# Kernel optimization log

Measured on AMD Instinct MI355X. Metric: run time of the kernel, lower is better.

Reference implementation:

```python
import jax, jax.numpy as jnp
import numpy as np

EPS = 1e-5

def _conv1x1(x, w, b):
    # x: [B, Din, N], w: [Dout, Din], b: [Dout]
    return jnp.einsum('od,bdn->bon', w, x) + b[None, :, None]

def _layernorm_last(x):
    # LayerNorm over last axis, no affine (matches torch LayerNorm([N], elementwise_affine=False))
    mu = jnp.mean(x, axis=-1, keepdims=True)
    var = jnp.mean(jnp.square(x - mu), axis=-1, keepdims=True)
    return (x - mu) * jax.lax.rsqrt(var + EPS)

def setup_inputs() -> dict:
    key = jax.random.key(0)
    ks = jax.random.split(key, 16)
    B, D, N, M = 1, 64, 64 * 80, 4096
    H2 = 2 * D
    s = 0.05
    return {
        'fea_pixel': jax.random.normal(ks[0], (B, D, N), jnp.float32),
        'fea_keypoint': jax.random.normal(ks[1], (B, D, M), jnp.float32),
        'Wq': jax.random.normal(ks[2], (D, D), jnp.float32) * s,
        'bq': jax.random.normal(ks[3], (D,), jnp.float32) * s,
        'Wk': jax.random.normal(ks[4], (D, D), jnp.float32) * s,
        'bk': jax.random.normal(ks[5], (D,), jnp.float32) * s,
        'Wv': jax.random.normal(ks[6], (D, D), jnp.float32) * s,
        'bv': jax.random.normal(ks[7], (D,), jnp.float32) * s,
        'Wm': jax.random.normal(ks[8], (D, D), jnp.float32) * s,
        'bm': jax.random.normal(ks[9], (D,), jnp.float32) * s,
        'W1': jax.random.normal(ks[10], (H2, D), jnp.float32) * s,
        'b1': jax.random.normal(ks[11], (H2,), jnp.float32) * s,
        'W2': jax.random.normal(ks[12], (D, H2), jnp.float32) * s,
        'b2': jax.random.normal(ks[13], (D,), jnp.float32) * s,
    }

def reference(fea_pixel, fea_keypoint, Wq, bq, Wk, bk, Wv, bv, Wm, bm, W1, b1, W2, b2):
    B, D, N = fea_pixel.shape
    num_heads = 4
    hd = D // num_heads  # head dim

    # QKV 1x1-conv projections, then split channels as (head_dim, num_heads) -- matches torch view
    q = _conv1x1(fea_pixel, Wq, bq).reshape(B, hd, num_heads, N)
    k = _conv1x1(fea_keypoint, Wk, bk).reshape(B, hd, num_heads, -1)
    v = _conv1x1(fea_keypoint, Wv, bv).reshape(B, hd, num_heads, -1)

    scores = jnp.einsum('bdhn,bdhm->bhnm', q, k) / jnp.sqrt(jnp.float32(hd))
    prob = jax.nn.softmax(scores, axis=-1)
    x = jnp.einsum('bhnm,bdhm->bdhn', prob, v)  # [B, hd, H, N]
    attn = _conv1x1(x.reshape(B, D, N), Wm, bm)

    fea = _layernorm_last(fea_pixel + attn)  # [B, D, N]

    # MLP over channel dim: operate on [B, N, D]
    y = jnp.swapaxes(fea, 1, 2)
    h = jax.nn.relu(jnp.einsum('bnd,od->bno', y, W1) + b1)
    m = jax.nn.relu(jnp.einsum('bno,do->bnd', h, W2) + b2)

    return _layernorm_last(fea + jnp.swapaxes(m, 1, 2))
```

## Files before the change

kernel.cpp:

```cpp
#include <hip/hip_runtime.h>
#include <hip/hip_bf16.h>

typedef __attribute__((ext_vector_type(4))) short short4v;
typedef __attribute__((ext_vector_type(4))) float float4v;

#define NHEADS 4
#define DMODEL 64
#define EPSV 1e-5f
#define QSCALE 0.36067376022224085f

__device__ inline short bf16rn(float f) {
    __hip_bfloat16 h = __float2bfloat16(f);
    return __builtin_bit_cast(short, h);
}

__device__ inline float exp2fast(float x) { return __builtin_amdgcn_exp2f(x); }

__global__ __launch_bounds__(512)
void proj_all_k(const float* __restrict__ Wk, const float* __restrict__ bk,
                const float* __restrict__ Wv, const float* __restrict__ bv,
                const float* __restrict__ Wq, const float* __restrict__ bq,
                const float* __restrict__ fkey, const float* __restrict__ fpix,
                short4v* __restrict__ kfrag, short4v* __restrict__ vfrag,
                short4v* __restrict__ qfrag, int M, int N) {
    __shared__ float xs[64][64];
    __shared__ float wsm[64][65];
    const int t = threadIdx.x;
    const int kvblocks = M >> 6;
    const bool isKV = (int)blockIdx.x < kvblocks;
    const int c0 = (isKV ? blockIdx.x : blockIdx.x - kvblocks) * 64;
    const float* x = isKV ? fkey : fpix;
    const int NC = isKV ? M : N;

    for (int i = t; i < 64 * 64; i += 512) {
        xs[i >> 6][i & 63] = x[(size_t)(i >> 6) * NC + c0 + (i & 63)];
        if (isKV) wsm[i >> 6][i & 63] = Wv[i];
    }
    __syncthreads();
    const int CT = NC >> 4;

    {
        const float* W = isKV ? Wk : Wq;
        const float* b = isKV ? bk : bq;
        const float scale = isKV ? 1.f : QSCALE;
        short4v* outf = isKV ? kfrag : qfrag;
        const int mm = t & 63;
        const int g8 = __builtin_amdgcn_readfirstlane(t >> 6);
        const int qd = g8 >> 1;
        const int half = g8 & 1;
        const int m = c0 + mm;
        float acc[8];
        #pragma unroll
        for (int a = 0; a < 8; ++a)
            acc[a] = b[qd * 16 + (a >> 1) * 4 + half * 2 + (a & 1)];
        #pragma unroll 8
        for (int d = 0; d < 64; ++d) {
            float xv = xs[d][mm];
            #pragma unroll
            for (int a = 0; a < 8; ++a)
                acc[a] = fmaf(W[(qd * 16 + (a >> 1) * 4 + half * 2 + (a & 1)) * 64 + d],
                              xv, acc[a]);
        }
        #pragma unroll
        for (int hh = 0; hh < 2; ++hh) {
            const int h = half * 2 + hh;
            short4v pk;
            #pragma unroll
            for (int j = 0; j < 4; ++j) pk[j] = bf16rn(acc[j * 2 + hh] * scale);
            outf[((size_t)(h * CT + (m >> 4))) * 64 + (m & 15) + 16 * qd] = pk;
        }
    }
    if (isKV) {
        const int lane = t & 63;
        const int w8 = t >> 6;
        const int d = lane >> 2, h = lane & 3;
        const float b0 = bv[lane];
        #pragma unroll
        for (int r = 0; r < 2; ++r) {
            const int mg = r * 8 + w8;
            float a0 = b0, a1 = b0, a2 = b0, a3 = b0;
            #pragma unroll 8
            for (int dd = 0; dd < 64; ++dd) {
                float wv = wsm[lane][dd];
                float4 xv = *(const float4*)&xs[dd][mg * 4];
                a0 = fmaf(wv, xv.x, a0); a1 = fmaf(wv, xv.y, a1);
                a2 = fmaf(wv, xv.z, a2); a3 = fmaf(wv, xv.w, a3);
            }
            short4v pk;
            pk[0] = bf16rn(a0); pk[1] = bf16rn(a1); pk[2] = bf16rn(a2); pk[3] = bf16rn(a3);
            const int m0 = c0 + mg * 4;
            vfrag[((size_t)(h * CT + (m0 >> 4))) * 64 + d + 16 * ((m0 >> 2) & 3)] = pk;
        }
    }
}

__global__ __launch_bounds__(256)
void attn_mfma_k(const short4v* __restrict__ qf, const short4v* __restrict__ kf,
                 const short4v* __restrict__ vf, float* __restrict__ xatt,
                 int N, int M) {
    const int lane = threadIdx.x & 63;
    const int ck = threadIdx.x >> 6;
    const int nt = blockIdx.x;
    const int h = blockIdx.y;
    const int NT = N >> 4, MT = M >> 4;
    const int mtN = MT >> 2;
    const int mt0 = ck * mtN;

    const short4v q4 = qf[((size_t)(h * NT + nt)) * 64 + lane];
    const float4v zero4 = {0.f, 0.f, 0.f, 0.f};
    float4v O = zero4;
    float ld = 0.f;
    const int g4 = (lane >> 4) << 2;

    const short4v* kp = kf + ((size_t)(h * MT + mt0)) * 64 + lane;
    const short4v* vp = vf + ((size_t)(h * MT + mt0)) * 64 + lane;
    for (int it = 0; it < mtN; it += 4) {
        short4v ka[4], va[4];
        #pragma unroll
        for (int u = 0; u < 4; ++u) {
            ka[u] = kp[(it + u) * 64];
            va[u] = vp[(it + u) * 64];
        }
        #pragma unroll
        for (int u = 0; u < 4; ++u) {
            float4v s = __builtin_amdgcn_mfma_f32_16x16x16bf16_1k(ka[u], q4, zero4, 0, 0, 0);
            float p0 = exp2fast(s[0]), p1 = exp2fast(s[1]),
                  p2 = exp2fast(s[2]), p3 = exp2fast(s[3]);
            ld += (p0 + p1) + (p2 + p3);
            short4v pa;
            pa[0] = bf16rn(p0); pa[1] = bf16rn(p1); pa[2] = bf16rn(p2); pa[3] = bf16rn(p3);
            O = __builtin_amdgcn_mfma_f32_16x16x16bf16_1k(pa, va[u], O, 0, 0, 0);
        }
    }
    ld += __shfl_xor(ld, 16);
    ld += __shfl_xor(ld, 32);

    __shared__ float Osm[4][256];
    __shared__ float lsm[4][16];
    #pragma unroll
    for (int b = 0; b < 4; ++b)
        Osm[ck][(g4 + b) * 16 + (lane & 15)] = O[b];
    if (lane < 16) lsm[ck][lane] = ld;
    __syncthreads();

    const int t = threadIdx.x;
    const int d = t >> 4, q = t & 15;
    const float L = (lsm[0][q] + lsm[1][q]) + (lsm[2][q] + lsm[3][q]);
    const int oi = q * 16 + d;
    const float val = (Osm[0][oi] + Osm[1][oi]) + (Osm[2][oi] + Osm[3][oi]);
    xatt[(size_t)(d * NHEADS + h) * N + nt * 16 + q] = val / L;
}

template<int DIN, int DOUT, bool RELU>
__global__ __launch_bounds__(256)
void conv1x1_k(const float* __restrict__ W, const float* __restrict__ bias,
               const float* __restrict__ x, float* __restrict__ out, int N) {
    __shared__ float xs[DIN][64];
    const int tid = threadIdx.x;
    const int n0 = blockIdx.x * 64;
    for (int i = tid; i < DIN * 64; i += 256) {
        int d = i >> 6, nn = i & 63;
        xs[d][nn] = x[(size_t)d * N + n0 + nn];
    }
    __syncthreads();
    const int nn = tid & 63;
    const int og = __builtin_amdgcn_readfirstlane((int)(threadIdx.x >> 6));
    const int ow = blockIdx.y * 16 + og * 4;
    float acc[4];
    #pragma unroll
    for (int i = 0; i < 4; ++i) acc[i] = bias[ow + i];
    #pragma unroll 8
    for (int d = 0; d < DIN; ++d) {
        float xv = xs[d][nn];
        #pragma unroll
        for (int i = 0; i < 4; ++i)
            acc[i] = fmaf(W[(ow + i) * DIN + d], xv, acc[i]);
    }
    #pragma unroll
    for (int i = 0; i < 4; ++i) {
        float r = RELU ? fmaxf(acc[i], 0.f) : acc[i];
        out[(size_t)(ow + i) * N + n0 + nn] = r;
    }
}

__global__ __launch_bounds__(512)
void add_ln_k(const float* __restrict__ a, const float* __restrict__ b,
              float* __restrict__ out, int N) {
    const int d = blockIdx.x;
    const int tid = threadIdx.x;
    const int nv = N >> 2;
    const float4* a4 = (const float4*)(a + (size_t)d * N);
    const float4* b4 = (const float4*)(b + (size_t)d * N);
    float4* o4 = (float4*)(out + (size_t)d * N);
    float s1 = 0.f, s2 = 0.f;
    for (int i = tid; i < nv; i += 512) {
        float4 va = a4[i], vb = b4[i];
        float tx = va.x + vb.x, ty = va.y + vb.y, tz = va.z + vb.z, tw = va.w + vb.w;
        s1 += (tx + ty) + (tz + tw);
        s2 = fmaf(tx, tx, s2); s2 = fmaf(ty, ty, s2);
        s2 = fmaf(tz, tz, s2); s2 = fmaf(tw, tw, s2);
    }
    #pragma unroll
    for (int m = 1; m < 64; m <<= 1) {
        s1 += __shfl_xor(s1, m);
        s2 += __shfl_xor(s2, m);
    }
    __shared__ float ws1[8], ws2[8];
    const int w = tid >> 6;
    if ((tid & 63) == 0) { ws1[w] = s1; ws2[w] = s2; }
    __syncthreads();
    s1 = 0.f; s2 = 0.f;
    #pragma unroll
    for (int i = 0; i < 8; ++i) { s1 += ws1[i]; s2 += ws2[i]; }
    const float mean = s1 / (float)N;
    const float var  = s2 / (float)N - mean * mean;
    const float rstd = rsqrtf(var + EPSV);
    for (int i = tid; i < nv; i += 512) {
        float4 va = a4[i], vb = b4[i];
        float4 r;
        r.x = (va.x + vb.x - mean) * rstd;
        r.y = (va.y + vb.y - mean) * rstd;
        r.z = (va.z + vb.z - mean) * rstd;
        r.w = (va.w + vb.w - mean) * rstd;
        o4[i] = r;
    }
}

extern "C" void kernel_launch(void* const* d_in, const int* in_sizes, int n_in,
                              void* d_out, int out_size, void* d_ws, size_t ws_size,
                              hipStream_t stream) {
    const float* fpix = (const float*)d_in[0];
    const float* fkey = (const float*)d_in[1];
    const float* Wq = (const float*)d_in[2];  const float* bq = (const float*)d_in[3];
    const float* Wk = (const float*)d_in[4];  const float* bk = (const float*)d_in[5];
    const float* Wv = (const float*)d_in[6];  const float* bv = (const float*)d_in[7];
    const float* Wm = (const float*)d_in[8];  const float* bm = (const float*)d_in[9];
    const float* W1 = (const float*)d_in[10]; const float* b1 = (const float*)d_in[11];
    const float* W2 = (const float*)d_in[12]; const float* b2 = (const float*)d_in[13];
    float* outp = (float*)d_out;

    const int N = in_sizes[0] / DMODEL;
    const int M = in_sizes[1] / DMODEL;

    char* wsb = (char*)d_ws;
    short4v* qfrag = (short4v*)(wsb);
    short4v* kfrag = (short4v*)(wsb + 655360);
    short4v* vfrag = (short4v*)(wsb + 1179648);
    float*   xatt  = (float*)(wsb + 1703936);
    float*   fea   = (float*)(wsb + 3014656);
    float*   attnb = (float*)(wsb + 4325376);
    float*   hbuf  = (float*)(wsb + 5636096);
    float*   mbuf  = (float*)(wsb + 8257536);

    proj_all_k<<<dim3(M / 64 + N / 64), 512, 0, stream>>>(Wk, bk, Wv, bv, Wq, bq,
                                                          fkey, fpix, kfrag, vfrag,
                                                          qfrag, M, N);
    attn_mfma_k<<<dim3(N / 16, NHEADS), 256, 0, stream>>>(qfrag, kfrag, vfrag, xatt, N, M);
    conv1x1_k<64, 64, false><<<dim3(N / 64, 4), 256, 0, stream>>>(Wm, bm, xatt, attnb, N);
    add_ln_k<<<64, 512, 0, stream>>>(fpix, attnb, fea, N);
    conv1x1_k<64, 128, true><<<dim3(N / 64, 8), 256, 0, stream>>>(W1, b1, fea, hbuf, N);
    conv1x1_k<128, 64, true><<<dim3(N / 64, 4), 256, 0, stream>>>(W2, b2, hbuf, mbuf, N);
    add_ln_k<<<64, 512, 0, stream>>>(fea, mbuf, outp, N);
}
```

Baseline: 62.36 us.

## Process two query tiles per wave in attention to reuse K/V fragments

Each wave in the attention kernel now computes two 16-row query tiles against the same K/V fragments, so every K/V load feeds four MFMAs instead of two. The block grows to 8 waves, each covering an eighth of the key range, and the grid halves along N. This cuts K/V memory traffic and adds independent MFMA work per iteration. In exchange it uses more registers and a larger shared-memory reduction over 8 partial sums.

Result: faster. 58.42 us (median of 2 runs) (-6.3%).

```diff
diff --git a/kernel.cpp b/kernel.cpp
--- a/kernel.cpp
+++ b/kernel.cpp
@@ -94,22 +94,23 @@
     }
 }
 
-__global__ __launch_bounds__(256)
+__global__ __launch_bounds__(512)
 void attn_mfma_k(const short4v* __restrict__ qf, const short4v* __restrict__ kf,
                  const short4v* __restrict__ vf, float* __restrict__ xatt,
                  int N, int M) {
     const int lane = threadIdx.x & 63;
     const int ck = threadIdx.x >> 6;
-    const int nt = blockIdx.x;
+    const int nt0 = blockIdx.x * 2;
     const int h = blockIdx.y;
     const int NT = N >> 4, MT = M >> 4;
-    const int mtN = MT >> 2;
+    const int mtN = MT >> 3;
     const int mt0 = ck * mtN;
 
-    const short4v q4 = qf[((size_t)(h * NT + nt)) * 64 + lane];
+    const short4v qa = qf[((size_t)(h * NT + nt0)) * 64 + lane];
+    const short4v qb = qf[((size_t)(h * NT + nt0 + 1)) * 64 + lane];
     const float4v zero4 = {0.f, 0.f, 0.f, 0.f};
-    float4v O = zero4;
-    float ld = 0.f;
+    float4v Oa = zero4, Ob = zero4;
+    float lda = 0.f, ldb = 0.f;
     const int g4 = (lane >> 4) << 2;
 
     const short4v* kp = kf + ((size_t)(h * MT + mt0)) * 64 + lane;
@@ -123,32 +124,48 @@
         }
         #pragma unroll
         for (int u = 0; u < 4; ++u) {
-            float4v s = __builtin_amdgcn_mfma_f32_16x16x16bf16_1k(ka[u], q4, zero4, 0, 0, 0);
-            float p0 = exp2fast(s[0]), p1 = exp2fast(s[1]),
-                  p2 = exp2fast(s[2]), p3 = exp2fast(s[3]);
-            ld += (p0 + p1) + (p2 + p3);
-            short4v pa;
-            pa[0] = bf16rn(p0); pa[1] = bf16rn(p1); pa[2] = bf16rn(p2); pa[3] = bf16rn(p3);
-            O = __builtin_amdgcn_mfma_f32_16x16x16bf16_1k(pa, va[u], O, 0, 0, 0);
-        }
-    }
-    ld += __shfl_xor(ld, 16);
-    ld += __shfl_xor(ld, 32);
-
-    __shared__ float Osm[4][256];
-    __shared__ float lsm[4][16];
-    #pragma unroll
-    for (int b = 0; b < 4; ++b)
-        Osm[ck][(g4 + b) * 16 + (lane & 15)] = O[b];
-    if (lane < 16) lsm[ck][lane] = ld;
+            float4v sa = __builtin_amdgcn_mfma_f32_16x16x16bf16_1k(ka[u], qa, zero4, 0, 0, 0);
+            float4v sb = __builtin_amdgcn_mfma_f32_16x16x16bf16_1k(ka[u], qb, zero4, 0, 0, 0);
+            float pa0 = exp2fast(sa[0]), pa1 = exp2fast(sa[1]),
+                  pa2 = exp2fast(sa[2]), pa3 = exp2fast(sa[3]);
+            float pb0 = exp2fast(sb[0]), pb1 = exp2fast(sb[1]),
+                  pb2 = exp2fast(sb[2]), pb3 = exp2fast(sb[3]);
+            lda += (pa0 + pa1) + (pa2 + pa3);
+            ldb += (pb0 + pb1) + (pb2 + pb3);
+            short4v fa, fb;
+            fa[0] = bf16rn(pa0); fa[1] = bf16rn(pa1); fa[2] = bf16rn(pa2); fa[3] = bf16rn(pa3);
+            fb[0] = bf16rn(pb0); fb[1] = bf16rn(pb1); fb[2] = bf16rn(pb2); fb[3] = bf16rn(pb3);
+            Oa = __builtin_amdgcn_mfma_f32_16x16x16bf16_1k(fa, va[u], Oa, 0, 0, 0);
+            Ob = __builtin_amdgcn_mfma_f32_16x16x16bf16_1k(fb, va[u], Ob, 0, 0, 0);
+        }
+    }
+    lda += __shfl_xor(lda, 16); lda += __shfl_xor(lda, 32);
+    ldb += __shfl_xor(ldb, 16); ldb += __shfl_xor(ldb, 32);
+
+    __shared__ float Osm[8][512];
+    __shared__ float lsm[8][32];
+    #pragma unroll
+    for (int b = 0; b < 4; ++b) {
+        Osm[ck][(g4 + b) * 16 + (lane & 15)]       = Oa[b];
+        Osm[ck][256 + (g4 + b) * 16 + (lane & 15)] = Ob[b];
+    }
+    if (lane < 16) {
+        lsm[ck][lane]      = lda;
+        lsm[ck][16 + lane] = ldb;
+    }
     __syncthreads();
 
     const int t = threadIdx.x;
-    const int d = t >> 4, q = t & 15;
-    const float L = (lsm[0][q] + lsm[1][q]) + (lsm[2][q] + lsm[3][q]);
-    const int oi = q * 16 + d;
-    const float val = (Osm[0][oi] + Osm[1][oi]) + (Osm[2][oi] + Osm[3][oi]);
-    xatt[(size_t)(d * NHEADS + h) * N + nt * 16 + q] = val / L;
+    const int j = t >> 8;
+    const int tt = t & 255;
+    const int d = tt >> 4, q = tt & 15;
+    float L = 0.f, val = 0.f;
+    #pragma unroll
+    for (int c = 0; c < 8; ++c) {
+        L   += lsm[c][j * 16 + q];
+        val += Osm[c][j * 256 + q * 16 + d];
+    }
+    xatt[(size_t)(d * NHEADS + h) * N + (nt0 + j) * 16 + q] = val / L;
 }
 
 template<int DIN, int DOUT, bool RELU>
@@ -255,7 +272,7 @@
     proj_all_k<<<dim3(M / 64 + N / 64), 512, 0, stream>>>(Wk, bk, Wv, bv, Wq, bq,
                                                           fkey, fpix, kfrag, vfrag,
                                                           qfrag, M, N);
-    attn_mfma_k<<<dim3(N / 16, NHEADS), 256, 0, stream>>>(qfrag, kfrag, vfrag, xatt, N, M);
+    attn_mfma_k<<<dim3(N / 32, NHEADS), 512, 0, stream>>>(qfrag, kfrag, vfrag, xatt, N, M);
     conv1x1_k<64, 64, false><<<dim3(N / 64, 4), 256, 0, stream>>>(Wm, bm, xatt, attnb, N);
     add_ln_k<<<64, 512, 0, stream>>>(fpix, attnb, fea, N);
     conv1x1_k<64, 128, true><<<dim3(N / 64, 8), 256, 0, stream>>>(W1, b1, fea, hbuf, N);
```
